# Kernel tuning notes

Measured on AMD Instinct MI355X. Metric: run time of the kernel, lower is better.

Reference implementation:

```python
import jax, jax.numpy as jnp
import numpy as np

# Dimensions: B walkers, NSPIN spins, NPS electrons per spin, DFEAT equivariant
# feature dim, NION ions, DSP spatial dim.
B, NSPIN, NPS, DFEAT, NION, DSP = 2048, 2, 8, 256, 4, 3


def setup_inputs() -> dict:
    key = jax.random.key(0)
    k0, k1, k2, k3, k4, k5 = jax.random.split(key, 6)
    eq_inputs = jax.random.normal(k0, (B, NSPIN * NPS, DFEAT), jnp.float32)
    r_ei = jax.random.normal(k1, (B, NSPIN * NPS, NION, DSP), jnp.float32)
    # Linear part of the orbitals: maps pair features (2*DFEAT) -> NPS orbitals per spin.
    W = jax.random.normal(k2, (NSPIN, 2 * DFEAT, NPS), jnp.float32) / np.sqrt(2.0 * DFEAT)
    b = 0.01 * jax.random.normal(k3, (NSPIN, NPS), jnp.float32)
    # Anisotropic decay: one DSPxDSP matrix per (spin, orbital, ion), near identity.
    env_dim = jnp.eye(DSP, dtype=jnp.float32)[None, None, None] + 0.05 * jax.random.normal(
        k4, (NSPIN, NPS, NION, DSP, DSP), jnp.float32
    )
    # Linear combination over ions per (spin, ion, orbital).
    env_ion = jnp.full((NSPIN, NION, NPS), 1.0 / NION, jnp.float32) + 0.05 * jax.random.normal(
        k5, (NSPIN, NION, NPS), jnp.float32
    )
    return {
        "eq_inputs": eq_inputs,
        "r_ei": r_ei,
        "W": W,
        "b": b,
        "env_dim": env_dim,
        "env_ion": env_ion,
    }


def reference(eq_inputs, r_ei, W, b, env_dim, env_ion):
    Bsz = eq_inputs.shape[0]
    # Split equally into spins: (B, NSPIN, NPS, DFEAT)
    x = eq_inputs.reshape(Bsz, NSPIN, NPS, DFEAT)
    # Doubly-equivariant pair features: concat(x_i, x_j) -> (B, S, n, n, 2d)
    shp = (Bsz, NSPIN, NPS, NPS, DFEAT)
    xi = jnp.broadcast_to(x[:, :, :, None, :], shp)
    xj = jnpp_concat = jnp.broadcast_to(x[:, :, None, :, :], shp)
    pairs = jnp.concatenate([xi, xj], axis=-1)
    # Linear part of the per-particle orbital matrices: (B, S, i, j, k)
    orb = jnp.einsum("bsijf,sfk->bsijk", pairs, W) + b[None, :, None, None, :]
    # Anisotropic exponential envelopes on the orbital-evaluated electron j:
    # env_{b,s,j,k} = sum_a env_ion[s,a,k] * exp(-||env_dim[s,k,a] @ r_ei[b,s,j,a]||)
    r = r_ei.reshape(Bsz, NSPIN, NPS, NION, DSP)
    scaled = jnp.einsum("bsjad,skade->bsjkae", r, env_dim)  # (B,S,j,k,a,e)
    dist = jnp.linalg.norm(scaled, axis=-1)  # (B,S,j,k,a)
    env = jnp.einsum("bsjka,sak->bsjk", jnp.exp(-dist), env_ion)
    orb = orb * env[:, :, None, :, :]
    # Per-particle determinants over the (j,k) axes: (B, S, n)
    dets = jnp.linalg.det(orb)[..., None]  # (B, S, n, 1)
    # Per-spin list, each (B, n, 1)
    return (dets[:, 0], dets[:, 1])
```

## Files before the change

### kernel.cpp

```cpp
#include <hip/hip_runtime.h>
#include <stdint.h>

#define BATCH 2048
#define NPS 8
#define DFEAT 256

typedef const float __attribute__((address_space(4))) cfp;
typedef __attribute__((address_space(3))) uint32_t lds_u32;
typedef const __attribute__((address_space(1))) uint32_t glb_u32;

__global__ __launch_bounds__(512) void ppdet_kernel(
    const float* __restrict__ eq,
    const float* __restrict__ r_ei,
    const float* __restrict__ W,
    const float* __restrict__ bias,
    const float* __restrict__ env_dim,
    const float* __restrict__ env_ion,
    float* __restrict__ out)
{
    __shared__ __align__(16) float X[4 * 64 * 64];
    __shared__ __align__(16) float AB[64 * 16];
    __shared__ __align__(16) float envl[512];
    float* part = X;

    const int tid = threadIdx.x;
    const int bid = blockIdx.x;
    const int s  = bid & 1;
    const int b0 = (bid >> 1) * 8;

    const int wq   = __builtin_amdgcn_readfirstlane(tid >> 6);
    const int lane = tid & 63;

    const int ew = tid >> 6, ek = (tid >> 3) & 7, ej = tid & 7;
    float4 ra, rb, rc;
    float md[4][9];
    float ei[4];
    {
        const size_t rrow = ((size_t)(b0 + ew) * 16 + s * 8 + ej) * 12;
        const float4* rp = (const float4*)(r_ei + rrow);
        ra = rp[0]; rb = rp[1]; rc = rp[2];
#pragma unroll
        for (int a = 0; a < 4; ++a) {
            const float* Md = env_dim + ((size_t)(s * 8 + ek) * 4 + a) * 9;
            const float4 m0 = *(const float4*)(Md);
            const float4 m1 = *(const float4*)(Md + 4);
            md[a][0] = m0.x; md[a][1] = m0.y; md[a][2] = m0.z; md[a][3] = m0.w;
            md[a][4] = m1.x; md[a][5] = m1.y; md[a][6] = m1.z; md[a][7] = m1.w;
            md[a][8] = Md[8];
            ei[a] = env_ion[(s * 4 + a) * 8 + ek];
        }
    }
    __builtin_amdgcn_sched_barrier(0);

    {
        const float* gw = eq + ((size_t)(b0 + wq) * 16 + s * 8) * DFEAT;
#pragma unroll
        for (int q = 0; q < 4; ++q) {
#pragma unroll
            for (int u = 0; u < 2; ++u) {
                const int r0 = wq * 8 + u * 4;
                const int r  = r0 + (lane >> 4);
                const int c  = (lane & 15) ^ ((r >> 1) & 7);
                const float* src = gw + (size_t)(r & 7) * DFEAT + q * 64 + c * 4;
                lds_u32* dst = (lds_u32*)(uintptr_t)&X[q * 4096 + r0 * 64];
                __builtin_amdgcn_global_load_lds((glb_u32*)src, dst, 16, 0, 0);
            }
            __builtin_amdgcn_sched_barrier(0);
        }
    }

    {
        float rr[12] = {ra.x, ra.y, ra.z, ra.w, rb.x, rb.y, rb.z, rb.w,
                        rc.x, rc.y, rc.z, rc.w};
        float e = 0.f;
#pragma unroll
        for (int a = 0; a < 4; ++a) {
            float r0 = rr[a * 3], r1 = rr[a * 3 + 1], r2 = rr[a * 3 + 2];
            float e0 = r0 * md[a][0] + r1 * md[a][3] + r2 * md[a][6];
            float e1 = r0 * md[a][1] + r1 * md[a][4] + r2 * md[a][7];
            float e2 = r0 * md[a][2] + r1 * md[a][5] + r2 * md[a][8];
            float dist = sqrtf(e0 * e0 + e1 * e1 + e2 * e2);
            e = fmaf(ei[a], __expf(-dist), e);
        }
        envl[ew * 64 + ej * 8 + ek] = e;
    }

    float acc[16];
#pragma unroll
    for (int k = 0; k < 16; ++k) acc[k] = 0.f;

    cfp* wbase = (cfp*)(uintptr_t)(W + s * 4096);
    const int perm = (lane >> 1) & 7;

#pragma unroll
    for (int h = 0; h < 2; ++h) {
        if (h == 0) asm volatile("s_waitcnt vmcnt(4)" ::: "memory");
        else        asm volatile("s_waitcnt vmcnt(0)" ::: "memory");
        __builtin_amdgcn_s_barrier();

#pragma unroll
        for (int qq = 0; qq < 2; ++qq) {
            const int q = h * 2 + qq;
            const float4 xa = *(const float4*)
                &X[q * 4096 + lane * 64 + (((2 * wq)     ^ perm) << 2)];
            const float4 xb = *(const float4*)
                &X[q * 4096 + lane * 64 + (((2 * wq + 1) ^ perm) << 2)];
            cfp* w1 = wbase + (q * 64 + wq * 8) * 8;
            const float xs[8] = {xa.x, xa.y, xa.z, xa.w, xb.x, xb.y, xb.z, xb.w};
#pragma unroll
            for (int i = 0; i < 8; ++i) {
                const float xc = xs[i];
#pragma unroll
                for (int k = 0; k < 8; ++k) {
                    acc[k]     = fmaf(xc, w1[i * 8 + k],        acc[k]);
                    acc[8 + k] = fmaf(xc, w1[2048 + i * 8 + k], acc[8 + k]);
                }
            }
        }
    }

    {
        float* pb = part + (wq * 64 + lane) * 16;
        const int sw = (lane >> 1) & 3;
#pragma unroll
        for (int kg = 0; kg < 4; ++kg) {
            int slot = kg ^ sw;
            float4 v = make_float4(acc[kg * 4], acc[kg * 4 + 1],
                                   acc[kg * 4 + 2], acc[kg * 4 + 3]);
            *(float4*)(pb + slot * 4) = v;
        }
    }

    __syncthreads();

    if (tid < 256) {
        const int row = tid >> 2, sl = tid & 3;
        const int g = sl ^ ((row >> 1) & 3);
        float4 sum = make_float4(0.f, 0.f, 0.f, 0.f);
#pragma unroll
        for (int q2 = 0; q2 < 8; ++q2) {
            float4 v = *(const float4*)(part + (q2 * 64 + row) * 16 + sl * 4);
            sum.x += v.x; sum.y += v.y; sum.z += v.z; sum.w += v.w;
        }
        if (g < 2) {
            sum.x += bias[s * 8 + g * 4];
            sum.y += bias[s * 8 + g * 4 + 1];
            sum.z += bias[s * 8 + g * 4 + 2];
            sum.w += bias[s * 8 + g * 4 + 3];
        }
        *(float4*)(AB + row * 16 + g * 4) = sum;
    }

    __syncthreads();

    if (tid < 64) {
        const int w = tid >> 3, i = tid & 7;
        float Arow[8];
#pragma unroll
        for (int k = 0; k < 8; ++k) Arow[k] = AB[(w * 8 + i) * 16 + k];
        float M[8][8];
#pragma unroll
        for (int j = 0; j < 8; ++j) {
#pragma unroll
            for (int k = 0; k < 8; ++k)
                M[j][k] = (Arow[k] + AB[(w * 8 + j) * 16 + 8 + k])
                          * envl[w * 64 + j * 8 + k];
        }
        float det = 1.f;
#pragma unroll
        for (int p = 0; p < 8; ++p) {
            int piv = p;
            float mx = fabsf(M[p][p]);
#pragma unroll
            for (int r2 = p + 1; r2 < 8; ++r2) {
                float v = fabsf(M[r2][p]);
                if (v > mx) { mx = v; piv = r2; }
            }
#pragma unroll
            for (int r2 = p + 1; r2 < 8; ++r2) {
                bool sw = (piv == r2);
#pragma unroll
                for (int c = p; c < 8; ++c) {
                    float a = M[p][c], bb = M[r2][c];
                    M[p][c]  = sw ? bb : a;
                    M[r2][c] = sw ? a : bb;
                }
            }
            det = (piv != p) ? -det : det;
            float d = M[p][p];
            det *= d;
            float inv = (d != 0.f) ? __builtin_amdgcn_rcpf(d) : 0.f;
#pragma unroll
            for (int r2 = p + 1; r2 < 8; ++r2) {
                float fct = M[r2][p] * inv;
#pragma unroll
                for (int c = p + 1; c < 8; ++c) M[r2][c] -= fct * M[p][c];
            }
        }
        out[(size_t)s * (BATCH * NPS) + (size_t)(b0 + w) * NPS + i] = det;
    }
}

extern "C" void kernel_launch(void* const* d_in, const int* in_sizes, int n_in,
                              void* d_out, int out_size, void* d_ws, size_t ws_size,
                              hipStream_t stream) {
    const float* eq      = (const float*)d_in[0];
    const float* r_ei    = (const float*)d_in[1];
    const float* W       = (const float*)d_in[2];
    const float* bias    = (const float*)d_in[3];
    const float* env_dim = (const float*)d_in[4];
    const float* env_ion = (const float*)d_in[5];
    float* out = (float*)d_out;

    ppdet_kernel<<<512, 512, 0, stream>>>(eq, r_ei, W, bias, env_dim, env_ion, out);
}
```

Before: 14.75 us.

## Process both spins per block with double-buffered LDS and staged waits

Each block now handles both spins for its 8 walkers instead of one, so the grid is halved to 256 blocks. Both spins' eq tiles are issued up front into separate LDS buffers, and staged vmcnt waits let spin-1 loads overlap spin-0 compute. The determinant step for both spins runs in one pass over 128 threads. The intent is to hide global load latency behind compute and amortize per-block setup, at the cost of doubled LDS use (about 140KB per block) and fewer blocks, which lowers parallelism and may limit occupancy.

```diff
diff --git a/kernel.cpp b/kernel.cpp
--- a/kernel.cpp
+++ b/kernel.cpp
@@ -18,42 +18,40 @@
     const float* __restrict__ env_ion,
     float* __restrict__ out)
 {
-    __shared__ __align__(16) float X[4 * 64 * 64];
-    __shared__ __align__(16) float AB[64 * 16];
-    __shared__ __align__(16) float envl[512];
-    float* part = X;
+    __shared__ __align__(16) float X[2][4 * 64 * 64];
+    __shared__ __align__(16) float AB[2][64 * 16];
+    __shared__ __align__(16) float envl[2][512];
 
     const int tid = threadIdx.x;
-    const int bid = blockIdx.x;
-    const int s  = bid & 1;
-    const int b0 = (bid >> 1) * 8;
+    const int b0 = blockIdx.x * 8;
 
     const int wq   = __builtin_amdgcn_readfirstlane(tid >> 6);
     const int lane = tid & 63;
 
     const int ew = tid >> 6, ek = (tid >> 3) & 7, ej = tid & 7;
-    float4 ra, rb, rc;
-    float md[4][9];
-    float ei[4];
-    {
-        const size_t rrow = ((size_t)(b0 + ew) * 16 + s * 8 + ej) * 12;
+    float4 ra0, rb0, rc0;
+    float md0[4][9];
+    float ei0[4];
+    {
+        const size_t rrow = ((size_t)(b0 + ew) * 16 + 0 * 8 + ej) * 12;
         const float4* rp = (const float4*)(r_ei + rrow);
-        ra = rp[0]; rb = rp[1]; rc = rp[2];
+        ra0 = rp[0]; rb0 = rp[1]; rc0 = rp[2];
 #pragma unroll
         for (int a = 0; a < 4; ++a) {
-            const float* Md = env_dim + ((size_t)(s * 8 + ek) * 4 + a) * 9;
+            const float* Md = env_dim + ((size_t)(0 * 8 + ek) * 4 + a) * 9;
             const float4 m0 = *(const float4*)(Md);
             const float4 m1 = *(const float4*)(Md + 4);
-            md[a][0] = m0.x; md[a][1] = m0.y; md[a][2] = m0.z; md[a][3] = m0.w;
-            md[a][4] = m1.x; md[a][5] = m1.y; md[a][6] = m1.z; md[a][7] = m1.w;
-            md[a][8] = Md[8];
-            ei[a] = env_ion[(s * 4 + a) * 8 + ek];
+            md0[a][0] = m0.x; md0[a][1] = m0.y; md0[a][2] = m0.z; md0[a][3] = m0.w;
+            md0[a][4] = m1.x; md0[a][5] = m1.y; md0[a][6] = m1.z; md0[a][7] = m1.w;
+            md0[a][8] = Md[8];
+            ei0[a] = env_ion[(0 * 4 + a) * 8 + ek];
         }
     }
     __builtin_amdgcn_sched_barrier(0);
 
-    {
-        const float* gw = eq + ((size_t)(b0 + wq) * 16 + s * 8) * DFEAT;
+#pragma unroll
+    for (int t = 0; t < 2; ++t) {
+        const float* gw = eq + ((size_t)(b0 + wq) * 16 + t * 8) * DFEAT;
 #pragma unroll
         for (int q = 0; q < 4; ++q) {
 #pragma unroll
@@ -62,7 +60,7 @@
                 const int r  = r0 + (lane >> 4);
                 const int c  = (lane & 15) ^ ((r >> 1) & 7);
                 const float* src = gw + (size_t)(r & 7) * DFEAT + q * 64 + c * 4;
-                lds_u32* dst = (lds_u32*)(uintptr_t)&X[q * 4096 + r0 * 64];
+                lds_u32* dst = (lds_u32*)(uintptr_t)&X[t][q * 4096 + r0 * 64];
                 __builtin_amdgcn_global_load_lds((glb_u32*)src, dst, 16, 0, 0);
             }
             __builtin_amdgcn_sched_barrier(0);
@@ -70,68 +68,80 @@
     }
 
     {
-        float rr[12] = {ra.x, ra.y, ra.z, ra.w, rb.x, rb.y, rb.z, rb.w,
-                        rc.x, rc.y, rc.z, rc.w};
+        float rr[12] = {ra0.x, ra0.y, ra0.z, ra0.w, rb0.x, rb0.y, rb0.z, rb0.w,
+                        rc0.x, rc0.y, rc0.z, rc0.w};
         float e = 0.f;
 #pragma unroll
         for (int a = 0; a < 4; ++a) {
             float r0 = rr[a * 3], r1 = rr[a * 3 + 1], r2 = rr[a * 3 + 2];
-            float e0 = r0 * md[a][0] + r1 * md[a][3] + r2 * md[a][6];
-            float e1 = r0 * md[a][1] + r1 * md[a][4] + r2 * md[a][7];
-            float e2 = r0 * md[a][2] + r1 * md[a][5] + r2 * md[a][8];
+            float e0 = r0 * md0[a][0] + r1 * md0[a][3] + r2 * md0[a][6];
+            float e1 = r0 * md0[a][1] + r1 * md0[a][4] + r2 * md0[a][7];
+            float e2 = r0 * md0[a][2] + r1 * md0[a][5] + r2 * md0[a][8];
             float dist = sqrtf(e0 * e0 + e1 * e1 + e2 * e2);
-            e = fmaf(ei[a], __expf(-dist), e);
-        }
-        envl[ew * 64 + ej * 8 + ek] = e;
-    }
-
+            e = fmaf(ei0[a], __expf(-dist), e);
+        }
+        envl[0][ew * 64 + ej * 8 + ek] = e;
+    }
+
+    const int perm = (lane >> 1) & 7;
     float acc[16];
 #pragma unroll
     for (int k = 0; k < 16; ++k) acc[k] = 0.f;
 
-    cfp* wbase = (cfp*)(uintptr_t)(W + s * 4096);
-    const int perm = (lane >> 1) & 7;
-
-#pragma unroll
-    for (int h = 0; h < 2; ++h) {
-        if (h == 0) asm volatile("s_waitcnt vmcnt(4)" ::: "memory");
-        else        asm volatile("s_waitcnt vmcnt(0)" ::: "memory");
-        __builtin_amdgcn_s_barrier();
-
-#pragma unroll
-        for (int qq = 0; qq < 2; ++qq) {
-            const int q = h * 2 + qq;
-            const float4 xa = *(const float4*)
-                &X[q * 4096 + lane * 64 + (((2 * wq)     ^ perm) << 2)];
-            const float4 xb = *(const float4*)
-                &X[q * 4096 + lane * 64 + (((2 * wq + 1) ^ perm) << 2)];
-            cfp* w1 = wbase + (q * 64 + wq * 8) * 8;
-            const float xs[8] = {xa.x, xa.y, xa.z, xa.w, xb.x, xb.y, xb.z, xb.w};
-#pragma unroll
-            for (int i = 0; i < 8; ++i) {
-                const float xc = xs[i];
-#pragma unroll
-                for (int k = 0; k < 8; ++k) {
-                    acc[k]     = fmaf(xc, w1[i * 8 + k],        acc[k]);
-                    acc[8 + k] = fmaf(xc, w1[2048 + i * 8 + k], acc[8 + k]);
-                }
-            }
-        }
-    }
-
-    {
-        float* pb = part + (wq * 64 + lane) * 16;
+    cfp* wbase0 = (cfp*)(uintptr_t)(W);
+    asm volatile("s_waitcnt vmcnt(12)" ::: "memory");
+    __builtin_amdgcn_s_barrier();
+#pragma unroll
+    for (int q = 0; q < 2; ++q) {
+        const float4 xa = *(const float4*)
+            &X[0][q * 4096 + lane * 64 + (((2 * wq)     ^ perm) << 2)];
+        const float4 xb = *(const float4*)
+            &X[0][q * 4096 + lane * 64 + (((2 * wq + 1) ^ perm) << 2)];
+        cfp* w1 = wbase0 + (q * 64 + wq * 8) * 8;
+        const float xs[8] = {xa.x, xa.y, xa.z, xa.w, xb.x, xb.y, xb.z, xb.w};
+#pragma unroll
+        for (int i = 0; i < 8; ++i) {
+            const float xc = xs[i];
+#pragma unroll
+            for (int k = 0; k < 8; ++k) {
+                acc[k]     = fmaf(xc, w1[i * 8 + k],        acc[k]);
+                acc[8 + k] = fmaf(xc, w1[2048 + i * 8 + k], acc[8 + k]);
+            }
+        }
+    }
+    asm volatile("s_waitcnt vmcnt(8)" ::: "memory");
+    __builtin_amdgcn_s_barrier();
+#pragma unroll
+    for (int q = 2; q < 4; ++q) {
+        const float4 xa = *(const float4*)
+            &X[0][q * 4096 + lane * 64 + (((2 * wq)     ^ perm) << 2)];
+        const float4 xb = *(const float4*)
+            &X[0][q * 4096 + lane * 64 + (((2 * wq + 1) ^ perm) << 2)];
+        cfp* w1 = wbase0 + (q * 64 + wq * 8) * 8;
+        const float xs[8] = {xa.x, xa.y, xa.z, xa.w, xb.x, xb.y, xb.z, xb.w};
+#pragma unroll
+        for (int i = 0; i < 8; ++i) {
+            const float xc = xs[i];
+#pragma unroll
+            for (int k = 0; k < 8; ++k) {
+                acc[k]     = fmaf(xc, w1[i * 8 + k],        acc[k]);
+                acc[8 + k] = fmaf(xc, w1[2048 + i * 8 + k], acc[8 + k]);
+            }
+        }
+    }
+
+    {
+        float* pb = &X[0][(wq * 64 + lane) * 16];
         const int sw = (lane >> 1) & 3;
 #pragma unroll
         for (int kg = 0; kg < 4; ++kg) {
             int slot = kg ^ sw;
-            float4 v = make_float4(acc[kg * 4], acc[kg * 4 + 1],
-                                   acc[kg * 4 + 2], acc[kg * 4 + 3]);
-            *(float4*)(pb + slot * 4) = v;
-        }
-    }
-
-    __syncthreads();
+            *(float4*)(pb + slot * 4) = make_float4(acc[kg * 4], acc[kg * 4 + 1],
+                                                    acc[kg * 4 + 2], acc[kg * 4 + 3]);
+        }
+    }
+    asm volatile("s_waitcnt lgkmcnt(0)" ::: "memory");
+    __builtin_amdgcn_s_barrier();
 
     if (tid < 256) {
         const int row = tid >> 2, sl = tid & 3;
@@ -139,32 +149,150 @@
         float4 sum = make_float4(0.f, 0.f, 0.f, 0.f);
 #pragma unroll
         for (int q2 = 0; q2 < 8; ++q2) {
-            float4 v = *(const float4*)(part + (q2 * 64 + row) * 16 + sl * 4);
+            float4 v = *(const float4*)&X[0][(q2 * 64 + row) * 16 + sl * 4];
             sum.x += v.x; sum.y += v.y; sum.z += v.z; sum.w += v.w;
         }
         if (g < 2) {
-            sum.x += bias[s * 8 + g * 4];
-            sum.y += bias[s * 8 + g * 4 + 1];
-            sum.z += bias[s * 8 + g * 4 + 2];
-            sum.w += bias[s * 8 + g * 4 + 3];
-        }
-        *(float4*)(AB + row * 16 + g * 4) = sum;
-    }
-
-    __syncthreads();
-
-    if (tid < 64) {
-        const int w = tid >> 3, i = tid & 7;
+            sum.x += bias[g * 4];
+            sum.y += bias[g * 4 + 1];
+            sum.z += bias[g * 4 + 2];
+            sum.w += bias[g * 4 + 3];
+        }
+        *(float4*)&AB[0][row * 16 + g * 4] = sum;
+    }
+
+#pragma unroll
+    for (int k = 0; k < 16; ++k) acc[k] = 0.f;
+    cfp* wbase1 = (cfp*)(uintptr_t)(W + 4096);
+
+    asm volatile("s_waitcnt vmcnt(4)" ::: "memory");
+    __builtin_amdgcn_s_barrier();
+#pragma unroll
+    for (int q = 0; q < 2; ++q) {
+        const float4 xa = *(const float4*)
+            &X[1][q * 4096 + lane * 64 + (((2 * wq)     ^ perm) << 2)];
+        const float4 xb = *(const float4*)
+            &X[1][q * 4096 + lane * 64 + (((2 * wq + 1) ^ perm) << 2)];
+        cfp* w1 = wbase1 + (q * 64 + wq * 8) * 8;
+        const float xs[8] = {xa.x, xa.y, xa.z, xa.w, xb.x, xb.y, xb.z, xb.w};
+#pragma unroll
+        for (int i = 0; i < 8; ++i) {
+            const float xc = xs[i];
+#pragma unroll
+            for (int k = 0; k < 8; ++k) {
+                acc[k]     = fmaf(xc, w1[i * 8 + k],        acc[k]);
+                acc[8 + k] = fmaf(xc, w1[2048 + i * 8 + k], acc[8 + k]);
+            }
+        }
+    }
+    asm volatile("s_waitcnt vmcnt(0)" ::: "memory");
+    __builtin_amdgcn_s_barrier();
+
+    float4 ra1, rb1, rc1;
+    float md1[4][9];
+    float ei1[4];
+    {
+        const size_t rrow = ((size_t)(b0 + ew) * 16 + 1 * 8 + ej) * 12;
+        const float4* rp = (const float4*)(r_ei + rrow);
+        ra1 = rp[0]; rb1 = rp[1]; rc1 = rp[2];
+#pragma unroll
+        for (int a = 0; a < 4; ++a) {
+            const float* Md = env_dim + ((size_t)(1 * 8 + ek) * 4 + a) * 9;
+            const float4 m0 = *(const float4*)(Md);
+            const float4 m1 = *(const float4*)(Md + 4);
+            md1[a][0] = m0.x; md1[a][1] = m0.y; md1[a][2] = m0.z; md1[a][3] = m0.w;
+            md1[a][4] = m1.x; md1[a][5] = m1.y; md1[a][6] = m1.z; md1[a][7] = m1.w;
+            md1[a][8] = Md[8];
+            ei1[a] = env_ion[(1 * 4 + a) * 8 + ek];
+        }
+    }
+
+#pragma unroll
+    for (int q = 2; q < 4; ++q) {
+        const float4 xa = *(const float4*)
+            &X[1][q * 4096 + lane * 64 + (((2 * wq)     ^ perm) << 2)];
+        const float4 xb = *(const float4*)
+            &X[1][q * 4096 + lane * 64 + (((2 * wq + 1) ^ perm) << 2)];
+        cfp* w1 = wbase1 + (q * 64 + wq * 8) * 8;
+        const float xs[8] = {xa.x, xa.y, xa.z, xa.w, xb.x, xb.y, xb.z, xb.w};
+#pragma unroll
+        for (int i = 0; i < 8; ++i) {
+            const float xc = xs[i];
+#pragma unroll
+            for (int k = 0; k < 8; ++k) {
+                acc[k]     = fmaf(xc, w1[i * 8 + k],        acc[k]);
+                acc[8 + k] = fmaf(xc, w1[2048 + i * 8 + k], acc[8 + k]);
+            }
+        }
+    }
+
+    {
+        float* pb = &X[1][(wq * 64 + lane) * 16];
+        const int sw = (lane >> 1) & 3;
+#pragma unroll
+        for (int kg = 0; kg < 4; ++kg) {
+            int slot = kg ^ sw;
+            *(float4*)(pb + slot * 4) = make_float4(acc[kg * 4], acc[kg * 4 + 1],
+                                                    acc[kg * 4 + 2], acc[kg * 4 + 3]);
+        }
+    }
+
+    {
+        float rr[12] = {ra1.x, ra1.y, ra1.z, ra1.w, rb1.x, rb1.y, rb1.z, rb1.w,
+                        rc1.x, rc1.y, rc1.z, rc1.w};
+        float e = 0.f;
+#pragma unroll
+        for (int a = 0; a < 4; ++a) {
+            float r0 = rr[a * 3], r1 = rr[a * 3 + 1], r2 = rr[a * 3 + 2];
+            float e0 = r0 * md1[a][0] + r1 * md1[a][3] + r2 * md1[a][6];
+            float e1 = r0 * md1[a][1] + r1 * md1[a][4] + r2 * md1[a][7];
+            float e2 = r0 * md1[a][2] + r1 * md1[a][5] + r2 * md1[a][8];
+            float dist = sqrtf(e0 * e0 + e1 * e1 + e2 * e2);
+            e = fmaf(ei1[a], __expf(-dist), e);
+        }
+        envl[1][ew * 64 + ej * 8 + ek] = e;
+    }
+
+    asm volatile("s_waitcnt lgkmcnt(0)" ::: "memory");
+    __builtin_amdgcn_s_barrier();
+
+    if (tid < 256) {
+        const int row = tid >> 2, sl = tid & 3;
+        const int g = sl ^ ((row >> 1) & 3);
+        float4 sum = make_float4(0.f, 0.f, 0.f, 0.f);
+#pragma unroll
+        for (int q2 = 0; q2 < 8; ++q2) {
+            float4 v = *(const float4*)&X[1][(q2 * 64 + row) * 16 + sl * 4];
+            sum.x += v.x; sum.y += v.y; sum.z += v.z; sum.w += v.w;
+        }
+        if (g < 2) {
+            sum.x += bias[8 + g * 4];
+            sum.y += bias[8 + g * 4 + 1];
+            sum.z += bias[8 + g * 4 + 2];
+            sum.w += bias[8 + g * 4 + 3];
+        }
+        *(float4*)&AB[1][row * 16 + g * 4] = sum;
+    }
+
+    asm volatile("s_waitcnt lgkmcnt(0)" ::: "memory");
+    __builtin_amdgcn_s_barrier();
+
+    if (tid < 128) {
+        const int t = tid >> 6;
+        const int l = tid & 63;
+        const int w = l >> 3, i = l & 7;
+        const float* ABt = AB[t];
+        const float* Et  = envl[t];
         float Arow[8];
 #pragma unroll
-        for (int k = 0; k < 8; ++k) Arow[k] = AB[(w * 8 + i) * 16 + k];
+        for (int k = 0; k < 8; ++k) Arow[k] = ABt[(w * 8 + i) * 16 + k];
         float M[8][8];
 #pragma unroll
         for (int j = 0; j < 8; ++j) {
 #pragma unroll
             for (int k = 0; k < 8; ++k)
-                M[j][k] = (Arow[k] + AB[(w * 8 + j) * 16 + 8 + k])
-                          * envl[w * 64 + j * 8 + k];
+                M[j][k] = (Arow[k] + ABt[(w * 8 + j) * 16 + 8 + k])
+                          * Et[w * 64 + j * 8 + k];
         }
         float det = 1.f;
 #pragma unroll
@@ -197,7 +325,7 @@
                 for (int c = p + 1; c < 8; ++c) M[r2][c] -= fct * M[p][c];
             }
         }
-        out[(size_t)s * (BATCH * NPS) + (size_t)(b0 + w) * NPS + i] = det;
+        out[(size_t)t * (BATCH * NPS) + (size_t)(b0 + w) * NPS + i] = det;
     }
 }
 
@@ -212,5 +340,5 @@
     const float* env_ion = (const float*)d_in[5];
     float* out = (float*)d_out;
 
-    ppdet_kernel<<<512, 512, 0, stream>>>(eq, r_ei, W, bias, env_dim, env_ion, out);
+    ppdet_kernel<<<256, 512, 0, stream>>>(eq, r_ei, W, bias, env_dim, env_ion, out);
 }
```

Result: slower. 18.43 us (+25.0%).

## Load half of eq features directly to registers, halving LDS staging buffer

Applied to the files above, without the earlier changes.

Only the first two of four feature quarters are now staged into LDS with async global-to-LDS loads. The last two quarters are loaded straight into registers with per-lane float4 global loads, and the wait counts are adjusted to match. This halves the shared-memory footprint, which may allow more resident blocks per CU, and removes LDS reads for half the GEMV. In exchange the direct loads are strided and less coalesced, and an extra barrier is added before the partial-sum area, which aliases X, is reused.

```diff
diff --git a/kernel.cpp b/kernel.cpp
--- a/kernel.cpp
+++ b/kernel.cpp
@@ -18,7 +18,7 @@
     const float* __restrict__ env_ion,
     float* __restrict__ out)
 {
-    __shared__ __align__(16) float X[4 * 64 * 64];
+    __shared__ __align__(16) float X[2 * 64 * 64];
     __shared__ __align__(16) float AB[64 * 16];
     __shared__ __align__(16) float envl[512];
     float* part = X;
@@ -55,7 +55,7 @@
     {
         const float* gw = eq + ((size_t)(b0 + wq) * 16 + s * 8) * DFEAT;
 #pragma unroll
-        for (int q = 0; q < 4; ++q) {
+        for (int q = 0; q < 2; ++q) {
 #pragma unroll
             for (int u = 0; u < 2; ++u) {
                 const int r0 = wq * 8 + u * 4;
@@ -69,6 +69,14 @@
         }
     }
 
+    const float* xr = eq
+        + ((size_t)(b0 + (lane >> 3)) * 16 + s * 8 + (lane & 7)) * DFEAT;
+    const float4 xg0 = *(const float4*)(xr + 128 + wq * 8);
+    const float4 xg1 = *(const float4*)(xr + 128 + wq * 8 + 4);
+    const float4 xg2 = *(const float4*)(xr + 192 + wq * 8);
+    const float4 xg3 = *(const float4*)(xr + 192 + wq * 8 + 4);
+    __builtin_amdgcn_sched_barrier(0);
+
     {
         float rr[12] = {ra.x, ra.y, ra.z, ra.w, rb.x, rb.y, rb.z, rb.w,
                         rc.x, rc.y, rc.z, rc.w};
@@ -84,6 +92,7 @@
         }
         envl[ew * 64 + ej * 8 + ek] = e;
     }
+    __builtin_amdgcn_sched_barrier(0);
 
     float acc[16];
 #pragma unroll
@@ -93,28 +102,44 @@
     const int perm = (lane >> 1) & 7;
 
 #pragma unroll
-    for (int h = 0; h < 2; ++h) {
-        if (h == 0) asm volatile("s_waitcnt vmcnt(4)" ::: "memory");
-        else        asm volatile("s_waitcnt vmcnt(0)" ::: "memory");
+    for (int q = 0; q < 2; ++q) {
+        if (q == 0) asm volatile("s_waitcnt vmcnt(6)" ::: "memory");
+        else        asm volatile("s_waitcnt vmcnt(4)" ::: "memory");
         __builtin_amdgcn_s_barrier();
 
-#pragma unroll
-        for (int qq = 0; qq < 2; ++qq) {
-            const int q = h * 2 + qq;
-            const float4 xa = *(const float4*)
-                &X[q * 4096 + lane * 64 + (((2 * wq)     ^ perm) << 2)];
-            const float4 xb = *(const float4*)
-                &X[q * 4096 + lane * 64 + (((2 * wq + 1) ^ perm) << 2)];
-            cfp* w1 = wbase + (q * 64 + wq * 8) * 8;
-            const float xs[8] = {xa.x, xa.y, xa.z, xa.w, xb.x, xb.y, xb.z, xb.w};
-#pragma unroll
-            for (int i = 0; i < 8; ++i) {
-                const float xc = xs[i];
-#pragma unroll
-                for (int k = 0; k < 8; ++k) {
-                    acc[k]     = fmaf(xc, w1[i * 8 + k],        acc[k]);
-                    acc[8 + k] = fmaf(xc, w1[2048 + i * 8 + k], acc[8 + k]);
-                }
+        const float4 xa = *(const float4*)
+            &X[q * 4096 + lane * 64 + (((2 * wq)     ^ perm) << 2)];
+        const float4 xb = *(const float4*)
+            &X[q * 4096 + lane * 64 + (((2 * wq + 1) ^ perm) << 2)];
+        cfp* w1 = wbase + (q * 64 + wq * 8) * 8;
+        const float xs[8] = {xa.x, xa.y, xa.z, xa.w, xb.x, xb.y, xb.z, xb.w};
+#pragma unroll
+        for (int i = 0; i < 8; ++i) {
+            const float xc = xs[i];
+#pragma unroll
+            for (int k = 0; k < 8; ++k) {
+                acc[k]     = fmaf(xc, w1[i * 8 + k],        acc[k]);
+                acc[8 + k] = fmaf(xc, w1[2048 + i * 8 + k], acc[8 + k]);
+            }
+        }
+    }
+
+    asm volatile("s_waitcnt lgkmcnt(0)" ::: "memory");
+    __builtin_amdgcn_s_barrier();
+
+#pragma unroll
+    for (int q = 2; q < 4; ++q) {
+        const float4 xa = (q == 2) ? xg0 : xg2;
+        const float4 xb = (q == 2) ? xg1 : xg3;
+        cfp* w1 = wbase + (q * 64 + wq * 8) * 8;
+        const float xs[8] = {xa.x, xa.y, xa.z, xa.w, xb.x, xb.y, xb.z, xb.w};
+#pragma unroll
+        for (int i = 0; i < 8; ++i) {
+            const float xc = xs[i];
+#pragma unroll
+            for (int k = 0; k < 8; ++k) {
+                acc[k]     = fmaf(xc, w1[i * 8 + k],        acc[k]);
+                acc[8 + k] = fmaf(xc, w1[2048 + i * 8 + k], acc[8 + k]);
             }
         }
     }
```

Result: slower. 15.66 us (+6.2%).
